# Kernel optimization log

Measured on AMD Instinct MI355X. Metric: run time of the kernel, lower is better.

The kernel has to match this reference:

```python
import jax, jax.numpy as jnp
import numpy as np

BATCH, K, DIM = 512, 65536, 768

def _l2norm(x, axis=-1, eps=1e-12):
    return x / jnp.maximum(jnp.linalg.norm(x, axis=axis, keepdims=True), eps)

def setup_inputs() -> dict:
    key = jax.random.key(0)
    ks = jax.random.split(key, 8)
    s = 1.0 / np.sqrt(2 * DIM)
    return {
        "img_features": jax.random.normal(ks[0], (BATCH, DIM), jnp.float32),
        "txt_features": jax.random.normal(ks[1], (BATCH, DIM), jnp.float32),
        # queue buffers are L2-normalized at init in the torch module
        "queue_img": _l2norm(jax.random.normal(ks[2], (K, DIM), jnp.float32)),
        "queue_txt": _l2norm(jax.random.normal(ks[3], (K, DIM), jnp.float32)),
        "W_diff": jax.random.normal(ks[4], (2 * DIM, DIM), jnp.float32) * s,
        "b_diff": jnp.zeros((DIM,), jnp.float32),
        "W_comb": jax.random.normal(ks[5], (2 * DIM, DIM), jnp.float32) * s,
        "b_comb": jnp.zeros((DIM,), jnp.float32),
        "logit_scale": jnp.full((1,), 100.0, jnp.float32),  # clip logit_scale.exp()
    }

def reference(img_features, txt_features, queue_img, queue_txt,
              W_diff, b_diff, W_comb, b_comb, logit_scale):
    # normalize encoder outputs
    img_f = _l2norm(img_features)          # [n, c]
    txt_f = _l2norm(txt_features)          # [n, c]
    # brute-force cosine retrieval against the text queue
    retrieval_mat = jnp.einsum('nc,kc->nk', img_f, queue_txt)  # [n, K]
    ind_similar = jnp.argmax(retrieval_mat, axis=-1)           # [n]
    t_similar = queue_txt[ind_similar]                          # gather [n, c]
    # diff_net_q: concat -> linear -> relu
    diff = jax.nn.relu(jnp.concatenate([txt_f, t_similar], -1) @ W_diff + b_diff)
    # combine_net_q: concat -> linear
    combined = jnp.concatenate([img_f, diff], -1) @ W_comb + b_comb
    scale = jnp.mean(logit_scale)
    logits = scale * jnp.einsum('nc,kc->nk', combined, queue_img)  # [n, K]
    # dequeue/enqueue: scatter batch rows into the queue at ptr=0
    new_queue_img = jax.lax.dynamic_update_slice(queue_img, img_f, (0, 0))
    new_queue_txt = jax.lax.dynamic_update_slice(queue_txt, txt_f, (0, 0))
    return logits, ind_similar, new_queue_img, new_queue_txt
```

## Files before the change

kernel.cpp:

```cpp
#include <hip/hip_runtime.h>
#include <stdint.h>
#include <stddef.h>

#define BATCH 512
#define NQ    65536
#define DIM   768
#define DIM2  1536
#define CONVB 2048

typedef __attribute__((ext_vector_type(4))) float f32x4;
typedef __attribute__((ext_vector_type(4))) unsigned short u16x4;
typedef __attribute__((ext_vector_type(8))) unsigned short u16x8;
typedef __attribute__((ext_vector_type(8))) __bf16 bf16x8;

static __device__ __forceinline__ unsigned short f2bf(float x){
    unsigned int u = __float_as_uint(x);
    unsigned int r = ((u >> 16) & 1u) + 0x7fffu;
    return (unsigned short)((u + r) >> 16);
}
static __device__ __forceinline__ float bf2f(unsigned short h){
    return __uint_as_float(((unsigned int)h) << 16);
}

struct T2 { float v1, v2; int i1, i2; };
static __device__ __forceinline__ void t2_add(T2& t, float v, int i){
    if (v > t.v1 || (v == t.v1 && i < t.i1)) { t.v2 = t.v1; t.i2 = t.i1; t.v1 = v; t.i1 = i; }
    else if (v > t.v2 || (v == t.v2 && i < t.i2)) { t.v2 = v; t.i2 = i; }
}
static __device__ __forceinline__ T2 t2_init(){ T2 t; t.v1 = -3.4e38f; t.v2 = -3.4e38f; t.i1 = 0x7fffffff; t.i2 = 0x7fffffff; return t; }

__global__ __launch_bounds__(256) void prep_all(
    const float* __restrict__ img, const float* __restrict__ txt,
    const float* __restrict__ qtxt, const float* __restrict__ qimg,
    const float* __restrict__ Wd, const float* __restrict__ Wc,
    unsigned short* __restrict__ bthi, unsigned short* __restrict__ bihi,
    float* __restrict__ img_f, float* __restrict__ txt_f,
    unsigned short* __restrict__ X2hi, unsigned short* __restrict__ X2lo,
    unsigned short* __restrict__ X1hi, unsigned short* __restrict__ X1lo,
    float* __restrict__ out2, float* __restrict__ out3,
    float* __restrict__ Td, float* __restrict__ Tc)
{
    __shared__ float tbuf[32][33];
    __shared__ float red[4];
    const int b = blockIdx.x;
    if (b < 2 * CONVB){
        const bool isT = (b < CONVB);
        const float* __restrict__ src = isT ? qtxt : qimg;
        float* __restrict__ dst = isT ? out3 : out2;
        unsigned short* __restrict__ hi = isT ? bthi : bihi;
        const int bb = isT ? b : b - CONVB;
        const size_t skip4 = (size_t)BATCH * DIM / 4;
        const size_t n4 = (size_t)NQ * DIM / 4;
        for (size_t i = (size_t)bb * 256 + threadIdx.x; i < n4; i += (size_t)CONVB * 256){
            f32x4 v = ((const f32x4*)src)[i];
            if (i >= skip4) __builtin_nontemporal_store(v, (f32x4*)dst + i);
            u16x4 h;
            #pragma unroll
            for (int j = 0; j < 4; j++) h[j] = f2bf(v[j]);
            *(u16x4*)(hi + 4*i) = h;
        }
    } else if (b < 2 * CONVB + 2 * BATCH){
        const int b2 = b - 2 * CONVB;
        const bool isimg = (b2 < BATCH);
        const int row = isimg ? b2 : b2 - BATCH;
        const float* src = (isimg ? img : txt) + (size_t)row * DIM;
        float v[3];
        float ss = 0.f;
        #pragma unroll
        for (int i = 0; i < 3; i++){ v[i] = src[threadIdx.x + i*256]; ss += v[i]*v[i]; }
        #pragma unroll
        for (int m = 1; m < 64; m <<= 1) ss += __shfl_xor(ss, m);
        if ((threadIdx.x & 63) == 0) red[threadIdx.x >> 6] = ss;
        __syncthreads();
        float tot = red[0] + red[1] + red[2] + red[3];
        float scale = 1.0f / fmaxf(sqrtf(tot), 1e-12f);
        float* fdst = (isimg ? img_f : txt_f) + (size_t)row * DIM;
        float* odst = (isimg ? out2  : out3 ) + (size_t)row * DIM;
        unsigned short* hid = (isimg ? X2hi : X1hi) + (size_t)row * DIM2;
        unsigned short* lod = (isimg ? X2lo : X1lo) + (size_t)row * DIM2;
        #pragma unroll
        for (int i = 0; i < 3; i++){
            int c = threadIdx.x + i*256;
            float y = v[i] * scale;
            fdst[c] = y; odst[c] = y;
            unsigned short h = f2bf(y);
            hid[c] = h; lod[c] = f2bf(y - bf2f(h));
        }
    } else {
        int t = b - 2 * CONVB - 2 * BATCH;
        const int z = t / 1152; t -= z * 1152;
        const int x = t % 24, y = t / 24;
        const float* W = z ? Wc : Wd;
        float*       T = z ? Tc : Td;
        const int x0 = x * 32, y0 = y * 32;
        const int tx = threadIdx.x & 31, ty = threadIdx.x >> 5;
        #pragma unroll
        for (int i = 0; i < 32; i += 8)
            tbuf[ty + i][tx] = W[(size_t)(y0 + ty + i) * DIM + x0 + tx];
        __syncthreads();
        #pragma unroll
        for (int i = 0; i < 32; i += 8)
            T[(size_t)(x0 + ty + i) * DIM2 + y0 + tx] = tbuf[tx][ty + i];
    }
}

#define EPI_TOP2      0
#define EPI_BIAS_RELU 1
#define EPI_BIAS      2
#define EPI_SCALE     3

template<int EPI>
__global__ __launch_bounds__(512, 2) void gemm_big(
    const unsigned short* __restrict__ Ahi, const unsigned short* __restrict__ Alo, int lda,
    const unsigned short* __restrict__ Bhi, const unsigned short* __restrict__ Blo, int ldb,
    int K, int Nout,
    float* __restrict__ outp, const float* __restrict__ scale_ptr, int Mtot)
{
    constexpr int NT = 512;
    constexpr int KS = 64;
    constexpr int HT = 16384;
    constexpr int BUF = 4 * HT;
    __shared__ __align__(16) char lds[2 * BUF];

    const int tid = threadIdx.x, lane = tid & 63, wid = tid >> 6;
    const int wm = wid >> 2, wn = wid & 3;
    const int lr = lane & 15, lg = lane >> 4;
    const int id = blockIdx.x;
    const int l  = (id & 7) * 64 + (id >> 3);
    const int nb = l >> 1, mb = l & 1;
    const int m0 = mb * 256, n0 = nb * 256;

    f32x4 acc[8][4] = {};

    auto stageHT = [&](int T){
        int kind = T & 3, ks = T >> 2;
        char* base = lds + (ks & 1) * BUF + kind * HT;
        const unsigned short* hi = (kind < 2) ? Ahi : Bhi;
        const unsigned short* lo = (kind < 2) ? Alo : Blo;
        int ld = (kind < 2) ? lda : ldb;
        int r0 = ((kind < 2) ? m0 : n0) + (kind & 1) * 128;
        int k0 = ks * KS;
        #pragma unroll
        for (int r = 0; r < 2; r++){
            int G = r * NT + tid, row = G >> 3, slot = G & 7, s0 = slot ^ (row & 7);
            const unsigned short* s = ((s0 < 4) ? hi : lo) + (size_t)(r0 + row) * ld + k0 + (s0 & 3) * 8;
            __builtin_amdgcn_global_load_lds(
                (const __attribute__((address_space(1))) void*)s,
                (__attribute__((address_space(3))) void*)(base + (r * NT + (tid & ~63)) * 16), 16, 0, 0);
        }
    };

    const int xh = (lg ^ (lr & 7)) << 4;
    const int xl = ((4 + lg) ^ (lr & 7)) << 4;

    const int nk = K / KS;
    stageHT(0); stageHT(1); stageHT(2); stageHT(3);
    if (nk > 1){
        stageHT(6); stageHT(7);
        asm volatile("s_waitcnt vmcnt(4)" ::: "memory");
    } else {
        asm volatile("s_waitcnt vmcnt(0)" ::: "memory");
    }
    __syncthreads();

    for (int kt = 0; kt < nk; kt++){
        const char* Ab = lds + (kt & 1) * BUF;
        const char* Bb = Ab + 2 * HT;
        bf16x8 bh[4], bl[4];
        #pragma unroll
        for (int q = 0; q < 4; q++){
            if (q < 2){ if (kt + 1 < nk) stageHT(4 * (kt + 1) + q); }
            else      { if (kt + 2 < nk) stageHT(4 * (kt + 2) + q); }
            if (q == 0){
                #pragma unroll
                for (int nf = 0; nf < 4; nf++){
                    const char* rp = Bb + (wn * 64 + nf * 16 + lr) * 128;
                    bh[nf] = *(const bf16x8*)(rp + xh);
                    bl[nf] = *(const bf16x8*)(rp + xl);
                }
            }
            const char* rp0 = Ab + (wm * 128 + q * 32 + lr) * 128;
            const char* rp1 = rp0 + 16 * 128;
            bf16x8 a0h = *(const bf16x8*)(rp0 + xh);
            bf16x8 a0l = *(const bf16x8*)(rp0 + xl);
            bf16x8 a1h = *(const bf16x8*)(rp1 + xh);
            bf16x8 a1l = *(const bf16x8*)(rp1 + xl);
            asm volatile("s_barrier" ::: "memory");
            asm volatile("s_waitcnt lgkmcnt(0)" ::: "memory");
            __builtin_amdgcn_sched_barrier(0);
            __builtin_amdgcn_s_setprio(1);
            #pragma unroll
            for (int nf = 0; nf < 4; nf++)
                acc[2*q  ][nf] = __builtin_amdgcn_mfma_f32_16x16x32_bf16(a0h, bh[nf], acc[2*q  ][nf], 0, 0, 0);
            #pragma unroll
            for (int nf = 0; nf < 4; nf++)
                acc[2*q+1][nf] = __builtin_amdgcn_mfma_f32_16x16x32_bf16(a1h, bh[nf], acc[2*q+1][nf], 0, 0, 0);
            #pragma unroll
            for (int nf = 0; nf < 4; nf++)
                acc[2*q  ][nf] = __builtin_amdgcn_mfma_f32_16x16x32_bf16(a0l, bl[nf], acc[2*q  ][nf], 0, 0, 0);
            #pragma unroll
            for (int nf = 0; nf < 4; nf++)
                acc[2*q+1][nf] = __builtin_amdgcn_mfma_f32_16x16x32_bf16(a1l, bl[nf], acc[2*q+1][nf], 0, 0, 0);
            __builtin_amdgcn_s_setprio(0);
            if (q == 3){
                if (kt < nk - 2)       asm volatile("s_waitcnt vmcnt(4)" ::: "memory");
                else if (kt == nk - 2) asm volatile("s_waitcnt vmcnt(0)" ::: "memory");
            }
            asm volatile("s_barrier" ::: "memory");
        }
    }

    if constexpr (EPI == EPI_TOP2){
        T2* t2l = (T2*)lds;
        #pragma unroll
        for (int mf = 0; mf < 8; mf++){
            #pragma unroll
            for (int r = 0; r < 4; r++){
                T2 t = t2_init();
                #pragma unroll
                for (int nf = 0; nf < 4; nf++){
                    int gc = n0 + wn * 64 + nf * 16 + lr;
                    t2_add(t, acc[mf][nf][r], gc);
                }
                #pragma unroll
                for (int m = 1; m < 16; m <<= 1){
                    float ov1 = __shfl_xor(t.v1, m), ov2 = __shfl_xor(t.v2, m);
                    int   oi1 = __shfl_xor(t.i1, m), oi2 = __shfl_xor(t.i2, m);
                    t2_add(t, ov1, oi1); t2_add(t, ov2, oi2);
                }
                if (lr == 0){
                    int rowit = wm * 128 + mf * 16 + lg * 4 + r;
                    t2l[wn * 256 + rowit] = t;
                }
            }
        }
        __syncthreads();
        if (tid < 256){
            T2 t = t2l[tid];
            #pragma unroll
            for (int w = 1; w < 4; w++){
                T2 o = t2l[w * 256 + tid];
                t2_add(t, o.v1, o.i1); t2_add(t, o.v2, o.i2);
            }
            f32x4 pk; pk[0] = t.v1; pk[1] = __int_as_float(t.i1); pk[2] = t.v2; pk[3] = __int_as_float(t.i2);
            ((f32x4*)outp)[(size_t)nb * Mtot + (m0 + tid)] = pk;
        }
    } else if constexpr (EPI == EPI_SCALE){
        float sc = scale_ptr[0];
        #pragma unroll
        for (int mf = 0; mf < 8; mf++)
        #pragma unroll
        for (int nf = 0; nf < 4; nf++)
        #pragma unroll
        for (int r = 0; r < 4; r++){
            int grow = m0 + wm * 128 + mf * 16 + lg * 4 + r;
            int gcol = n0 + wn * 64 + nf * 16 + lr;
            outp[(size_t)grow * Nout + gcol] = acc[mf][nf][r] * sc;
        }
    }
}

template<int BM,int BN,int WGM,int WGN,int EPI>
__global__ __launch_bounds__(WGM*WGN*64) void gemm_small(
    const unsigned short* __restrict__ Ahi, const unsigned short* __restrict__ Alo, int lda,
    const float* __restrict__ B, int ldb, int K,
    const float* __restrict__ bias,
    unsigned short* __restrict__ dsthi, unsigned short* __restrict__ dstlo, int ldd, int dstoff)
{
    constexpr int WM = BM / WGM, WN = BN / WGN;
    constexpr int MF = WM / 16, NF = WN / 16;
    constexpr int NT = WGM * WGN * 64;
    constexpr int ABYTES = BM * 128;
    constexpr int BBYTES = BN * 128;
    constexpr int BUF = ABYTES + BBYTES;
    static_assert(BN * 4 == NT, "");
    static_assert((BM * 8) % NT == 0, "");

    __shared__ __align__(16) char lds[2 * BUF];

    const int tid  = threadIdx.x;
    const int wid  = tid >> 6, lane = tid & 63;
    const int wm   = wid / WGN, wn = wid % WGN;
    const int lr   = lane & 15, lg = lane >> 4;
    const int nb   = blockIdx.x, mb = blockIdx.y;
    const int m0   = mb * BM, n0 = nb * BN;

    f32x4 acc[MF][NF] = {};
    f32x4 breg0, breg1;

    auto stageA = [&](int buf, int k0){
        char* base = lds + buf * BUF;
        constexpr int RA = BM * 8 / NT;
        #pragma unroll
        for (int r = 0; r < RA; r++){
            int G = r * NT + tid;
            int row = G >> 3, slot = G & 7;
            int s0 = slot ^ (row & 7);
            const unsigned short* src = ((s0 < 4) ? Ahi : Alo)
                + (size_t)(m0 + row) * lda + (k0 + (s0 & 3) * 8);
            char* ldst = base + r * NT * 16 + (tid & ~63) * 16;
            __builtin_amdgcn_global_load_lds(
                (const __attribute__((address_space(1))) void*)src,
                (__attribute__((address_space(3))) void*)ldst, 16, 0, 0);
        }
    };
    auto loadB = [&](int kt){
        int k0 = kt * 32;
        int row = tid >> 2, quad = tid & 3;
        const float* bp = B + (size_t)(n0 + row) * ldb + k0 + quad * 8;
        breg0 = *(const f32x4*)bp;
        breg1 = *(const f32x4*)(bp + 4);
    };
    auto writeB = [&](int buf){
        char* base = lds + buf * BUF + ABYTES;
        int row = tid >> 2, quad = tid & 3;
        u16x8 h8, l8;
        #pragma unroll
        for (int j = 0; j < 8; j++){
            float x = (j < 4) ? breg0[j] : breg1[j - 4];
            unsigned short h = f2bf(x);
            h8[j] = h; l8[j] = f2bf(x - bf2f(h));
        }
        int sh = quad ^ (row & 7), sl = (4 + quad) ^ (row & 7);
        *(u16x8*)(base + row * 128 + sh * 16) = h8;
        *(u16x8*)(base + row * 128 + sl * 16) = l8;
    };
    auto compute = [&](int buf){
        const char* Ab = lds + buf * BUF;
        const char* Bb = Ab + ABYTES;
        bf16x8 ah[MF], al[MF], bh[NF], bl[NF];
        #pragma unroll
        for (int mf = 0; mf < MF; mf++){
            int row = wm * WM + mf * 16 + lr;
            const char* rp = Ab + row * 128;
            ah[mf] = *(const bf16x8*)(rp + ((lg ^ (row & 7)) << 4));
            al[mf] = *(const bf16x8*)(rp + (((4 + lg) ^ (row & 7)) << 4));
        }
        #pragma unroll
        for (int nf = 0; nf < NF; nf++){
            int row = wn * WN + nf * 16 + lr;
            const char* rp = Bb + row * 128;
            bh[nf] = *(const bf16x8*)(rp + ((lg ^ (row & 7)) << 4));
            bl[nf] = *(const bf16x8*)(rp + (((4 + lg) ^ (row & 7)) << 4));
        }
        #pragma unroll
        for (int mf = 0; mf < MF; mf++)
        #pragma unroll
        for (int nf = 0; nf < NF; nf++){
            acc[mf][nf] = __builtin_amdgcn_mfma_f32_16x16x32_bf16(ah[mf], bh[nf], acc[mf][nf], 0, 0, 0);
            acc[mf][nf] = __builtin_amdgcn_mfma_f32_16x16x32_bf16(al[mf], bh[nf], acc[mf][nf], 0, 0, 0);
            acc[mf][nf] = __builtin_amdgcn_mfma_f32_16x16x32_bf16(ah[mf], bl[nf], acc[mf][nf], 0, 0, 0);
        }
    };

    stageA(0, 0); loadB(0); writeB(0);
    __syncthreads();
    const int nk = K / 32;
    int cur = 0;
    for (int kt = 0; kt < nk; kt++){
        if (kt + 1 < nk){ stageA(cur ^ 1, (kt + 1) * 32); loadB(kt + 1); }
        compute(cur);
        if (kt + 1 < nk){ writeB(cur ^ 1); }
        __syncthreads();
        cur ^= 1;
    }

    #pragma unroll
    for (int mf = 0; mf < MF; mf++)
    #pragma unroll
    for (int nf = 0; nf < NF; nf++)
    #pragma unroll
    for (int r = 0; r < 4; r++){
        int grow = m0 + wm * WM + mf * 16 + lg * 4 + r;
        int gcol = n0 + wn * WN + nf * 16 + lr;
        float c = acc[mf][nf][r] + bias[gcol];
        if (EPI == EPI_BIAS_RELU) c = fmaxf(c, 0.f);
        unsigned short h = f2bf(c);
        size_t o = (size_t)grow * ldd + dstoff + gcol;
        dsthi[o] = h;
        dstlo[o] = f2bf(c - bf2f(h));
    }
}

__global__ __launch_bounds__(256) void phaseB_kernel(
    const f32x4* __restrict__ top2ws, int ntiles,
    const float* __restrict__ img_f, const float* __restrict__ qtxt,
    float* __restrict__ out_ind,
    unsigned short* __restrict__ X1hi, unsigned short* __restrict__ X1lo)
{
    __shared__ float vals[512];
    __shared__ int   inds[512];
    __shared__ float red[4];
    __shared__ int   redi[4];
    __shared__ int   cands[4];
    __shared__ float cscore[4];
    __shared__ int   finali;
    const int row = blockIdx.x, tid = threadIdx.x;

    if (tid < ntiles){
        f32x4 e = top2ws[(size_t)tid * BATCH + row];
        vals[2*tid]   = e[0]; inds[2*tid]   = __float_as_int(e[1]);
        vals[2*tid+1] = e[2]; inds[2*tid+1] = __float_as_int(e[3]);
    }
    __syncthreads();

    for (int it = 0; it < 4; it++){
        float v = vals[tid]; int i = inds[tid];
        {
            float v2 = vals[tid+256]; int i2 = inds[tid+256];
            if (v2 > v || (v2 == v && i2 < i)){ v = v2; i = i2; }
        }
        #pragma unroll
        for (int m = 1; m < 64; m <<= 1){
            float ov = __shfl_xor(v, m); int oi = __shfl_xor(i, m);
            if (ov > v || (ov == v && oi < i)){ v = ov; i = oi; }
        }
        if ((tid & 63) == 0){ red[tid>>6] = v; redi[tid>>6] = i; }
        __syncthreads();
        if (tid == 0){
            float bv = red[0]; int bi = redi[0];
            #pragma unroll
            for (int w = 1; w < 4; w++)
                if (red[w] > bv || (red[w] == bv && redi[w] < bi)){ bv = red[w]; bi = redi[w]; }
            cands[it] = bi;
        }
        __syncthreads();
        if (inds[tid]     == cands[it]) vals[tid]     = -3.4e38f;
        if (inds[tid+256] == cands[it]) vals[tid+256] = -3.4e38f;
        __syncthreads();
    }

    const float* a = img_f + (size_t)row * DIM;
    float a0 = a[tid], a1 = a[tid + 256], a2 = a[tid + 512];
    for (int c = 0; c < 4; c++){
        const float* bp = qtxt + (size_t)cands[c] * DIM;
        float s = a0 * bp[tid] + a1 * bp[tid + 256] + a2 * bp[tid + 512];
        #pragma unroll
        for (int m = 1; m < 64; m <<= 1) s += __shfl_xor(s, m);
        if ((tid & 63) == 0) red[tid>>6] = s;
        __syncthreads();
        if (tid == 0) cscore[c] = red[0] + red[1] + red[2] + red[3];
        __syncthreads();
    }
    if (tid == 0){
        float bs = cscore[0]; int bi = cands[0];
        #pragma unroll
        for (int c = 1; c < 4; c++)
            if (cscore[c] > bs || (cscore[c] == bs && cands[c] < bi)){ bs = cscore[c]; bi = cands[c]; }
        out_ind[row] = (float)bi;
        finali = bi;
    }
    __syncthreads();

    const float* src = qtxt + (size_t)finali * DIM;
    for (int c = tid; c < DIM; c += 256){
        float x = src[c];
        unsigned short h = f2bf(x);
        X1hi[(size_t)row * DIM2 + DIM + c] = h;
        X1lo[(size_t)row * DIM2 + DIM + c] = f2bf(x - bf2f(h));
    }
}

extern "C" void kernel_launch(void* const* d_in, const int* in_sizes, int n_in,
                              void* d_out, int out_size, void* d_ws, size_t ws_size,
                              hipStream_t stream)
{
    (void)in_sizes; (void)n_in; (void)out_size; (void)ws_size;
    const float* img  = (const float*)d_in[0];
    const float* txt  = (const float*)d_in[1];
    const float* qimg = (const float*)d_in[2];
    const float* qtxt = (const float*)d_in[3];
    const float* Wd   = (const float*)d_in[4];
    const float* bd   = (const float*)d_in[5];
    const float* Wc   = (const float*)d_in[6];
    const float* bc   = (const float*)d_in[7];
    const float* ls   = (const float*)d_in[8];

    float* out0 = (float*)d_out;
    float* out1 = out0 + (size_t)BATCH * NQ;
    float* out2 = out1 + BATCH;
    float* out3 = out2 + (size_t)NQ * DIM;

    char* w = (char*)d_ws;
    auto alloc = [&](size_t bytes){ char* p = w; w += (bytes + 255) & ~(size_t)255; return p; };
    unsigned short* X1hi  = (unsigned short*)alloc((size_t)BATCH * DIM2 * 2);
    unsigned short* X1lo  = (unsigned short*)alloc((size_t)BATCH * DIM2 * 2);
    unsigned short* X2hi  = (unsigned short*)alloc((size_t)BATCH * DIM2 * 2);
    unsigned short* X2lo  = (unsigned short*)alloc((size_t)BATCH * DIM2 * 2);
    unsigned short* combhi= (unsigned short*)alloc((size_t)BATCH * DIM * 2);
    unsigned short* comblo= (unsigned short*)alloc((size_t)BATCH * DIM * 2);
    float* img_f  = (float*)alloc((size_t)BATCH * DIM * 4);
    float* txt_f  = (float*)alloc((size_t)BATCH * DIM * 4);
    float* Td     = (float*)alloc((size_t)DIM * DIM2 * 4);
    float* Tc     = (float*)alloc((size_t)DIM * DIM2 * 4);
    float* top2ws = (float*)alloc((size_t)(NQ / 256) * BATCH * 16);
    unsigned short* Bt_hi = (unsigned short*)alloc((size_t)NQ * DIM * 2);
    unsigned short* Bi_hi = (unsigned short*)alloc((size_t)NQ * DIM * 2);

    prep_all<<<dim3(2 * CONVB + 2 * BATCH + 2304), dim3(256), 0, stream>>>(
        img, txt, qtxt, qimg, Wd, Wc, Bt_hi, Bi_hi,
        img_f, txt_f, X2hi, X2lo, X1hi, X1lo, out2, out3, Td, Tc);

    gemm_big<EPI_TOP2><<<dim3(512), dim3(512), 0, stream>>>(
        X2hi, X2hi + 32, DIM2, Bt_hi, Bt_hi + 32, DIM, DIM, NQ, top2ws, nullptr, BATCH);

    phaseB_kernel<<<dim3(BATCH), dim3(256), 0, stream>>>(
        (const f32x4*)top2ws, NQ / 256, img_f, qtxt, out1, X1hi, X1lo);

    gemm_small<64,64,2,2,EPI_BIAS_RELU><<<dim3(DIM / 64, BATCH / 64), dim3(256), 0, stream>>>(
        X1hi, X1lo, DIM2, Td, DIM2, DIM2, bd, X2hi, X2lo, DIM2, DIM);

    gemm_small<64,64,2,2,EPI_BIAS><<<dim3(DIM / 64, BATCH / 64), dim3(256), 0, stream>>>(
        X2hi, X2lo, DIM2, Tc, DIM2, DIM2, bc, combhi, comblo, DIM, 0);

    gemm_big<EPI_SCALE><<<dim3(512), dim3(512), 0, stream>>>(
        combhi, combhi + 32, DIM, Bi_hi, Bi_hi + 32, DIM, DIM, NQ, out0, ls, BATCH);
}
```

Measured before the change: 459.2 us.

## Overlap queue conversion/copy with GEMMs via extra producer warps

Moves the qimg fp32-to-bf16 conversion and the queue_img copy out of the prep kernel into two extra wavefronts of the first big GEMM. It also moves the queue_txt copy into two extra wavefronts of the second big GEMM. Those warps stream the data in phases synchronized with the GEMM's barriers, hiding memory traffic behind MFMA compute. The cost is launch bounds going from 512x2 to 640x1, which halves blocks per CU and may hurt GEMM latency hiding. The extra loads and stores also compete with GEMM operand bandwidth.

```diff
diff --git a/kernel.cpp b/kernel.cpp
--- a/kernel.cpp
+++ b/kernel.cpp
@@ -31,9 +31,9 @@
 
 __global__ __launch_bounds__(256) void prep_all(
     const float* __restrict__ img, const float* __restrict__ txt,
-    const float* __restrict__ qtxt, const float* __restrict__ qimg,
+    const float* __restrict__ qtxt,
     const float* __restrict__ Wd, const float* __restrict__ Wc,
-    unsigned short* __restrict__ bthi, unsigned short* __restrict__ bihi,
+    unsigned short* __restrict__ bthi,
     float* __restrict__ img_f, float* __restrict__ txt_f,
     unsigned short* __restrict__ X2hi, unsigned short* __restrict__ X2lo,
     unsigned short* __restrict__ X1hi, unsigned short* __restrict__ X1lo,
@@ -43,24 +43,17 @@
     __shared__ float tbuf[32][33];
     __shared__ float red[4];
     const int b = blockIdx.x;
-    if (b < 2 * CONVB){
-        const bool isT = (b < CONVB);
-        const float* __restrict__ src = isT ? qtxt : qimg;
-        float* __restrict__ dst = isT ? out3 : out2;
-        unsigned short* __restrict__ hi = isT ? bthi : bihi;
-        const int bb = isT ? b : b - CONVB;
-        const size_t skip4 = (size_t)BATCH * DIM / 4;
+    if (b < CONVB){
         const size_t n4 = (size_t)NQ * DIM / 4;
-        for (size_t i = (size_t)bb * 256 + threadIdx.x; i < n4; i += (size_t)CONVB * 256){
-            f32x4 v = ((const f32x4*)src)[i];
-            if (i >= skip4) __builtin_nontemporal_store(v, (f32x4*)dst + i);
+        for (size_t i = (size_t)b * 256 + threadIdx.x; i < n4; i += (size_t)CONVB * 256){
+            f32x4 v = ((const f32x4*)qtxt)[i];
             u16x4 h;
             #pragma unroll
             for (int j = 0; j < 4; j++) h[j] = f2bf(v[j]);
-            *(u16x4*)(hi + 4*i) = h;
-        }
-    } else if (b < 2 * CONVB + 2 * BATCH){
-        const int b2 = b - 2 * CONVB;
+            *(u16x4*)(bthi + 4*i) = h;
+        }
+    } else if (b < CONVB + 2 * BATCH){
+        const int b2 = b - CONVB;
         const bool isimg = (b2 < BATCH);
         const int row = isimg ? b2 : b2 - BATCH;
         const float* src = (isimg ? img : txt) + (size_t)row * DIM;
@@ -87,7 +80,7 @@
             hid[c] = h; lod[c] = f2bf(y - bf2f(h));
         }
     } else {
-        int t = b - 2 * CONVB - 2 * BATCH;
+        int t = b - CONVB - 2 * BATCH;
         const int z = t / 1152; t -= z * 1152;
         const int x = t % 24, y = t / 24;
         const float* W = z ? Wc : Wd;
@@ -110,153 +103,194 @@
 #define EPI_SCALE     3
 
 template<int EPI>
-__global__ __launch_bounds__(512, 2) void gemm_big(
+__global__ __launch_bounds__(640, 1) void gemm_big(
     const unsigned short* __restrict__ Ahi, const unsigned short* __restrict__ Alo, int lda,
     const unsigned short* __restrict__ Bhi, const unsigned short* __restrict__ Blo, int ldb,
     int K, int Nout,
-    float* __restrict__ outp, const float* __restrict__ scale_ptr, int Mtot)
+    float* __restrict__ outp, const float* __restrict__ scale_ptr, int Mtot,
+    const float* __restrict__ cv_src, unsigned short* __restrict__ cv_bf,
+    float* __restrict__ cv_fp)
 {
-    constexpr int NT = 512;
+    constexpr int STG = 512;
     constexpr int KS = 64;
     constexpr int HT = 16384;
     constexpr int BUF = 4 * HT;
     __shared__ __align__(16) char lds[2 * BUF];
 
     const int tid = threadIdx.x, lane = tid & 63, wid = tid >> 6;
-    const int wm = wid >> 2, wn = wid & 3;
-    const int lr = lane & 15, lg = lane >> 4;
-    const int id = blockIdx.x;
-    const int l  = (id & 7) * 64 + (id >> 3);
-    const int nb = l >> 1, mb = l & 1;
-    const int m0 = mb * 256, n0 = nb * 256;
-
-    f32x4 acc[8][4] = {};
-
-    auto stageHT = [&](int T){
-        int kind = T & 3, ks = T >> 2;
-        char* base = lds + (ks & 1) * BUF + kind * HT;
-        const unsigned short* hi = (kind < 2) ? Ahi : Bhi;
-        const unsigned short* lo = (kind < 2) ? Alo : Blo;
-        int ld = (kind < 2) ? lda : ldb;
-        int r0 = ((kind < 2) ? m0 : n0) + (kind & 1) * 128;
-        int k0 = ks * KS;
-        #pragma unroll
-        for (int r = 0; r < 2; r++){
-            int G = r * NT + tid, row = G >> 3, slot = G & 7, s0 = slot ^ (row & 7);
-            const unsigned short* s = ((s0 < 4) ? hi : lo) + (size_t)(r0 + row) * ld + k0 + (s0 & 3) * 8;
-            __builtin_amdgcn_global_load_lds(
-                (const __attribute__((address_space(1))) void*)s,
-                (__attribute__((address_space(3))) void*)(base + (r * NT + (tid & ~63)) * 16), 16, 0, 0);
-        }
-    };
-
-    const int xh = (lg ^ (lr & 7)) << 4;
-    const int xl = ((4 + lg) ^ (lr & 7)) << 4;
-
     const int nk = K / KS;
-    stageHT(0); stageHT(1); stageHT(2); stageHT(3);
-    if (nk > 1){
-        stageHT(6); stageHT(7);
-        asm volatile("s_waitcnt vmcnt(4)" ::: "memory");
-    } else {
-        asm volatile("s_waitcnt vmcnt(0)" ::: "memory");
-    }
-    __syncthreads();
-
-    for (int kt = 0; kt < nk; kt++){
-        const char* Ab = lds + (kt & 1) * BUF;
-        const char* Bb = Ab + 2 * HT;
-        bf16x8 bh[4], bl[4];
-        #pragma unroll
-        for (int q = 0; q < 4; q++){
-            if (q < 2){ if (kt + 1 < nk) stageHT(4 * (kt + 1) + q); }
-            else      { if (kt + 2 < nk) stageHT(4 * (kt + 2) + q); }
-            if (q == 0){
+
+    if (wid < 8){
+        const int wm = wid >> 2, wn = wid & 3;
+        const int lr = lane & 15, lg = lane >> 4;
+        const int id = blockIdx.x;
+        const int l  = (id & 7) * 64 + (id >> 3);
+        const int nb = l >> 1, mb = l & 1;
+        const int m0 = mb * 256, n0 = nb * 256;
+
+        f32x4 acc[8][4] = {};
+
+        auto stageHT = [&](int T){
+            int kind = T & 3, ks = T >> 2;
+            char* base = lds + (ks & 1) * BUF + kind * HT;
+            const unsigned short* hi = (kind < 2) ? Ahi : Bhi;
+            const unsigned short* lo = (kind < 2) ? Alo : Blo;
+            int ld = (kind < 2) ? lda : ldb;
+            int r0 = ((kind < 2) ? m0 : n0) + (kind & 1) * 128;
+            int k0 = ks * KS;
+            #pragma unroll
+            for (int r = 0; r < 2; r++){
+                int G = r * STG + tid, row = G >> 3, slot = G & 7, s0 = slot ^ (row & 7);
+                const unsigned short* s = ((s0 < 4) ? hi : lo) + (size_t)(r0 + row) * ld + k0 + (s0 & 3) * 8;
+                __builtin_amdgcn_global_load_lds(
+                    (const __attribute__((address_space(1))) void*)s,
+                    (__attribute__((address_space(3))) void*)(base + (r * STG + (tid & ~63)) * 16), 16, 0, 0);
+            }
+        };
+
+        const int xh = (lg ^ (lr & 7)) << 4;
+        const int xl = ((4 + lg) ^ (lr & 7)) << 4;
+
+        stageHT(0); stageHT(1); stageHT(2); stageHT(3);
+        if (nk > 1){
+            stageHT(6); stageHT(7);
+            asm volatile("s_waitcnt vmcnt(4)" ::: "memory");
+        } else {
+            asm volatile("s_waitcnt vmcnt(0)" ::: "memory");
+        }
+        __builtin_amdgcn_s_barrier();
+
+        for (int kt = 0; kt < nk; kt++){
+            const char* Ab = lds + (kt & 1) * BUF;
+            const char* Bb = Ab + 2 * HT;
+            bf16x8 bh[4], bl[4];
+            #pragma unroll
+            for (int q = 0; q < 4; q++){
+                if (q < 2){ if (kt + 1 < nk) stageHT(4 * (kt + 1) + q); }
+                else      { if (kt + 2 < nk) stageHT(4 * (kt + 2) + q); }
+                if (q == 0){
+                    #pragma unroll
+                    for (int nf = 0; nf < 4; nf++){
+                        const char* rp = Bb + (wn * 64 + nf * 16 + lr) * 128;
+                        bh[nf] = *(const bf16x8*)(rp + xh);
+                        bl[nf] = *(const bf16x8*)(rp + xl);
+                    }
+                }
+                const char* rp0 = Ab + (wm * 128 + q * 32 + lr) * 128;
+                const char* rp1 = rp0 + 16 * 128;
+                bf16x8 a0h = *(const bf16x8*)(rp0 + xh);
+                bf16x8 a0l = *(const bf16x8*)(rp0 + xl);
+                bf16x8 a1h = *(const bf16x8*)(rp1 + xh);
+                bf16x8 a1l = *(const bf16x8*)(rp1 + xl);
+                asm volatile("s_barrier" ::: "memory");
+                asm volatile("s_waitcnt lgkmcnt(0)" ::: "memory");
+                __builtin_amdgcn_sched_barrier(0);
+                __builtin_amdgcn_s_setprio(1);
                 #pragma unroll
-                for (int nf = 0; nf < 4; nf++){
-                    const char* rp = Bb + (wn * 64 + nf * 16 + lr) * 128;
-                    bh[nf] = *(const bf16x8*)(rp + xh);
-                    bl[nf] = *(const bf16x8*)(rp + xl);
+                for (int nf = 0; nf < 4; nf++)
+                    acc[2*q  ][nf] = __builtin_amdgcn_mfma_f32_16x16x32_bf16(a0h, bh[nf], acc[2*q  ][nf], 0, 0, 0);
+                #pragma unroll
+                for (int nf = 0; nf < 4; nf++)
+                    acc[2*q+1][nf] = __builtin_amdgcn_mfma_f32_16x16x32_bf16(a1h, bh[nf], acc[2*q+1][nf], 0, 0, 0);
+                #pragma unroll
+                for (int nf = 0; nf < 4; nf++)
+                    acc[2*q  ][nf] = __builtin_amdgcn_mfma_f32_16x16x32_bf16(a0l, bl[nf], acc[2*q  ][nf], 0, 0, 0);
+                #pragma unroll
+                for (int nf = 0; nf < 4; nf++)
+                    acc[2*q+1][nf] = __builtin_amdgcn_mfma_f32_16x16x32_bf16(a1l, bl[nf], acc[2*q+1][nf], 0, 0, 0);
+                __builtin_amdgcn_s_setprio(0);
+                if (q == 3){
+                    if (kt < nk - 2)       asm volatile("s_waitcnt vmcnt(4)" ::: "memory");
+                    else if (kt == nk - 2) asm volatile("s_waitcnt vmcnt(0)" ::: "memory");
+                }
+                asm volatile("s_barrier" ::: "memory");
+            }
+        }
+
+        if constexpr (EPI == EPI_TOP2){
+            T2* t2l = (T2*)lds;
+            #pragma unroll
+            for (int mf = 0; mf < 8; mf++){
+                #pragma unroll
+                for (int r = 0; r < 4; r++){
+                    T2 t = t2_init();
+                    #pragma unroll
+                    for (int nf = 0; nf < 4; nf++){
+                        int gc = n0 + wn * 64 + nf * 16 + lr;
+                        t2_add(t, acc[mf][nf][r], gc);
+                    }
+                    #pragma unroll
+                    for (int m = 1; m < 16; m <<= 1){
+                        float ov1 = __shfl_xor(t.v1, m), ov2 = __shfl_xor(t.v2, m);
+                        int   oi1 = __shfl_xor(t.i1, m), oi2 = __shfl_xor(t.i2, m);
+                        t2_add(t, ov1, oi1); t2_add(t, ov2, oi2);
+                    }
+                    if (lr == 0){
+                        int rowit = wm * 128 + mf * 16 + lg * 4 + r;
+                        t2l[wn * 256 + rowit] = t;
+                    }
                 }
             }
-            const char* rp0 = Ab + (wm * 128 + q * 32 + lr) * 128;
-            const char* rp1 = rp0 + 16 * 128;
-            bf16x8 a0h = *(const bf16x8*)(rp0 + xh);
-            bf16x8 a0l = *(const bf16x8*)(rp0 + xl);
-            bf16x8 a1h = *(const bf16x8*)(rp1 + xh);
-            bf16x8 a1l = *(const bf16x8*)(rp1 + xl);
-            asm volatile("s_barrier" ::: "memory");
             asm volatile("s_waitcnt lgkmcnt(0)" ::: "memory");
-            __builtin_amdgcn_sched_barrier(0);
-            __builtin_amdgcn_s_setprio(1);
+            __builtin_amdgcn_s_barrier();
+            if (tid < 256){
+                T2 t = t2l[tid];
+                #pragma unroll
+                for (int w = 1; w < 4; w++){
+                    T2 o = t2l[w * 256 + tid];
+                    t2_add(t, o.v1, o.i1); t2_add(t, o.v2, o.i2);
+                }
+                f32x4 pk; pk[0] = t.v1; pk[1] = __int_as_float(t.i1); pk[2] = t.v2; pk[3] = __int_as_float(t.i2);
+                ((f32x4*)outp)[(size_t)nb * Mtot + (m0 + tid)] = pk;
+            }
+        } else if constexpr (EPI == EPI_SCALE){
+            float sc = scale_ptr[0];
+            #pragma unroll
+            for (int mf = 0; mf < 8; mf++)
             #pragma unroll
             for (int nf = 0; nf < 4; nf++)
-                acc[2*q  ][nf] = __builtin_amdgcn_mfma_f32_16x16x32_bf16(a0h, bh[nf], acc[2*q  ][nf], 0, 0, 0);
-            #pragma unroll
-            for (int nf = 0; nf < 4; nf++)
-                acc[2*q+1][nf] = __builtin_amdgcn_mfma_f32_16x16x32_bf16(a1h, bh[nf], acc[2*q+1][nf], 0, 0, 0);
-            #pragma unroll
-            for (int nf = 0; nf < 4; nf++)
-                acc[2*q  ][nf] = __builtin_amdgcn_mfma_f32_16x16x32_bf16(a0l, bl[nf], acc[2*q  ][nf], 0, 0, 0);
-            #pragma unroll
-            for (int nf = 0; nf < 4; nf++)
-                acc[2*q+1][nf] = __builtin_amdgcn_mfma_f32_16x16x32_bf16(a1l, bl[nf], acc[2*q+1][nf], 0, 0, 0);
-            __builtin_amdgcn_s_setprio(0);
-            if (q == 3){
-                if (kt < nk - 2)       asm volatile("s_waitcnt vmcnt(4)" ::: "memory");
-                else if (kt == nk - 2) asm volatile("s_waitcnt vmcnt(0)" ::: "memory");
+            #pragma unroll
+            for (int r = 0; r < 4; r++){
+                int grow = m0 + wm * 128 + mf * 16 + lg * 4 + r;
+                int gcol = n0 + wn * 64 + nf * 16 + lr;
+                outp[(size_t)grow * Nout + gcol] = acc[mf][nf][r] * sc;
             }
-            asm volatile("s_barrier" ::: "memory");
-        }
-    }
-
-    if constexpr (EPI == EPI_TOP2){
-        T2* t2l = (T2*)lds;
-        #pragma unroll
-        for (int mf = 0; mf < 8; mf++){
-            #pragma unroll
-            for (int r = 0; r < 4; r++){
-                T2 t = t2_init();
-                #pragma unroll
-                for (int nf = 0; nf < 4; nf++){
-                    int gc = n0 + wn * 64 + nf * 16 + lr;
-                    t2_add(t, acc[mf][nf][r], gc);
+        }
+    } else {
+        const int cw = wid - 8;
+        const size_t base = ((size_t)blockIdx.x * 2 + cw) * 64 + lane;
+        const size_t stride = (size_t)512 * 2 * 64;
+        const size_t skip = (size_t)BATCH * DIM / 4;
+        f32x4 v[2][4];
+        auto issue = [&](int buf, int p){
+            #pragma unroll
+            for (int s = 0; s < 4; s++)
+                v[buf][s] = __builtin_nontemporal_load((const f32x4*)cv_src + base + (size_t)(4*p + s) * stride);
+        };
+        auto flush = [&](int buf, int p){
+            #pragma unroll
+            for (int s = 0; s < 4; s++){
+                size_t idx = base + (size_t)(4*p + s) * stride;
+                if (cv_bf){
+                    u16x4 h;
+                    #pragma unroll
+                    for (int j = 0; j < 4; j++) h[j] = f2bf(v[buf][s][j]);
+                    *(u16x4*)(cv_bf + 4*idx) = h;
                 }
-                #pragma unroll
-                for (int m = 1; m < 16; m <<= 1){
-                    float ov1 = __shfl_xor(t.v1, m), ov2 = __shfl_xor(t.v2, m);
-                    int   oi1 = __shfl_xor(t.i1, m), oi2 = __shfl_xor(t.i2, m);
-                    t2_add(t, ov1, oi1); t2_add(t, ov2, oi2);
-                }
-                if (lr == 0){
-                    int rowit = wm * 128 + mf * 16 + lg * 4 + r;
-                    t2l[wn * 256 + rowit] = t;
-                }
+                if (idx >= skip)
+                    __builtin_nontemporal_store(v[buf][s], (f32x4*)cv_fp + idx);
             }
-        }
-        __syncthreads();
-        if (tid < 256){
-            T2 t = t2l[tid];
-            #pragma unroll
-            for (int w = 1; w < 4; w++){
-                T2 o = t2l[w * 256 + tid];
-                t2_add(t, o.v1, o.i1); t2_add(t, o.v2, o.i2);
-            }
-            f32x4 pk; pk[0] = t.v1; pk[1] = __int_as_float(t.i1); pk[2] = t.v2; pk[3] = __int_as_float(t.i2);
-            ((f32x4*)outp)[(size_t)nb * Mtot + (m0 + tid)] = pk;
-        }
-    } else if constexpr (EPI == EPI_SCALE){
-        float sc = scale_ptr[0];
-        #pragma unroll
-        for (int mf = 0; mf < 8; mf++)
-        #pragma unroll
-        for (int nf = 0; nf < 4; nf++)
-        #pragma unroll
-        for (int r = 0; r < 4; r++){
-            int grow = m0 + wm * 128 + mf * 16 + lg * 4 + r;
-            int gcol = n0 + wn * 64 + nf * 16 + lr;
-            outp[(size_t)grow * Nout + gcol] = acc[mf][nf][r] * sc;
-        }
+        };
+        issue(0, 0);
+        __builtin_amdgcn_s_barrier();
+        const int nph = nk * 4;
+        for (int p = 0; p < nph; p++){
+            if (p + 1 < nph) issue((p + 1) & 1, p + 1);
+            flush(p & 1, p);
+            __builtin_amdgcn_s_barrier();
+            __builtin_amdgcn_s_barrier();
+        }
+        if (EPI == EPI_TOP2) __builtin_amdgcn_s_barrier();
     }
 }
 
@@ -497,12 +531,13 @@
     unsigned short* Bt_hi = (unsigned short*)alloc((size_t)NQ * DIM * 2);
     unsigned short* Bi_hi = (unsigned short*)alloc((size_t)NQ * DIM * 2);
 
-    prep_all<<<dim3(2 * CONVB + 2 * BATCH + 2304), dim3(256), 0, stream>>>(
-        img, txt, qtxt, qimg, Wd, Wc, Bt_hi, Bi_hi,
+    prep_all<<<dim3(CONVB + 2 * BATCH + 2304), dim3(256), 0, stream>>>(
+        img, txt, qtxt, Wd, Wc, Bt_hi,
         img_f, txt_f, X2hi, X2lo, X1hi, X1lo, out2, out3, Td, Tc);
 
-    gemm_big<EPI_TOP2><<<dim3(512), dim3(512), 0, stream>>>(
-        X2hi, X2hi + 32, DIM2, Bt_hi, Bt_hi + 32, DIM, DIM, NQ, top2ws, nullptr, BATCH);
+    gemm_big<EPI_TOP2><<<dim3(512), dim3(640), 0, stream>>>(
+        X2hi, X2hi + 32, DIM2, Bt_hi, Bt_hi + 32, DIM, DIM, NQ, top2ws, nullptr, BATCH,
+        qimg, Bi_hi, out2);
 
     phaseB_kernel<<<dim3(BATCH), dim3(256), 0, stream>>>(
         (const f32x4*)top2ws, NQ / 256, img_f, qtxt, out1, X1hi, X1lo);
@@ -513,6 +548,7 @@
     gemm_small<64,64,2,2,EPI_BIAS><<<dim3(DIM / 64, BATCH / 64), dim3(256), 0, stream>>>(
         X2hi, X2lo, DIM2, Tc, DIM2, DIM2, bc, combhi, comblo, DIM, 0);
 
-    gemm_big<EPI_SCALE><<<dim3(512), dim3(512), 0, stream>>>(
-        combhi, combhi + 32, DIM, Bi_hi, Bi_hi + 32, DIM, DIM, NQ, out0, ls, BATCH);
-}
+    gemm_big<EPI_SCALE><<<dim3(512), dim3(640), 0, stream>>>(
+        combhi, combhi + 32, DIM, Bi_hi, Bi_hi + 32, DIM, DIM, NQ, out0, ls, BATCH,
+        qtxt, (unsigned short*)nullptr, out3);
+}
```

Result: slower. 1.180 ms (+156.9%).
